# Kernel tuning notes

Hardware: AMD Instinct MI355X
Metric: run time of the kernel (lower is better)

The kernel has to match this reference:

```python
import jax, jax.numpy as jnp
import numpy as np

NEG_INF = -1.0e9  # matches torch masked_fill value of -1e9


def setup_inputs() -> dict:
    key = jax.random.key(0)
    ks = jax.random.split(key, 9)
    B, N, d, dh, de = 8, 512, 256, 64, 32
    x = jax.random.normal(ks[0], (B, N, d), dtype=jnp.float32)
    e = jax.random.normal(ks[1], (B, N, N, de), dtype=jnp.float32)
    node_mask = jax.random.randint(ks[2], (B, N), 0, 2, dtype=jnp.int32)
    Wq = jax.random.normal(ks[3], (d, dh), dtype=jnp.float32) / np.sqrt(d)
    bq = jax.random.normal(ks[4], (dh,), dtype=jnp.float32) * 0.02
    Wk = jax.random.normal(ks[5], (d, dh), dtype=jnp.float32) / np.sqrt(d)
    bk = jax.random.normal(ks[6], (dh,), dtype=jnp.float32) * 0.02
    Wv = jax.random.normal(ks[7], (d, dh), dtype=jnp.float32) / np.sqrt(d)
    bv = jax.random.normal(ks[8], (dh,), dtype=jnp.float32) * 0.02
    return {"x": x, "e": e, "node_mask": node_mask,
            "Wq": Wq, "bq": bq, "Wk": Wk, "bk": bk, "Wv": Wv, "bv": bv}


def reference(x, e, node_mask, Wq, bq, Wk, bk, Wv, bv):
    # x: (B,N,d), node_mask: (B,N) in {0,1}
    x_mask = node_mask.astype(x.dtype)[..., None]          # (B,N,1)
    Q = (x @ Wq + bq) * x_mask                              # (B,N,dh)
    K = (x @ Wk + bk) * x_mask
    V = (x @ Wv + bv) * x_mask
    sqrt_d = jnp.sqrt(jnp.asarray(Q.shape[-1], dtype=x.dtype))
    Att = jnp.einsum('bid,bjd->bij', Q, K) / sqrt_d        # (B,N,N)
    att_mask = (node_mask[:, :, None] * node_mask[:, None, :]).astype(bool)
    Att = jnp.where(att_mask, Att, NEG_INF)
    Att = jax.nn.softmax(Att, axis=-1)
    # dropout with p=0.0 is the identity
    out = jnp.einsum('bij,bjd->bid', Att, V) * x_mask       # (B,N,dh)
    return (out, e)
```

## Files before the change

kernel.cpp:

```cpp
#include <hip/hip_runtime.h>

#define B 8
#define N 512
#define D 256
#define DH 64
#define NEG_INF (-1.0e9f)
#define ROWS 8

#define ATTN_BLOCKS (B * N)
#define COPY_BLOCKS 8192
#define COPY_F4     (B * (size_t)N * N * 32 / 4)
#define COPY_ITERS  (COPY_F4 / ((size_t)COPY_BLOCKS * 256))

__global__ __launch_bounds__(192) void qkv_kernel(
    const float* __restrict__ x, const int* __restrict__ mask,
    const float* __restrict__ Wq, const float* __restrict__ bq,
    const float* __restrict__ Wk, const float* __restrict__ bk,
    const float* __restrict__ Wv, const float* __restrict__ bv,
    float* __restrict__ Q, float* __restrict__ K, float* __restrict__ V)
{
    __shared__ float xs[ROWS * D];
    const int tid  = threadIdx.x;
    const int row0 = blockIdx.x * ROWS;

    const float4* x4  = (const float4*)(x + (size_t)row0 * D);
    float4*       xs4 = (float4*)xs;
    for (int i = tid; i < ROWS * D / 4; i += 192) xs4[i] = x4[i];
    __syncthreads();

    const int which = tid >> 6;
    const int o     = tid & 63;
    const float* W    = (which == 0) ? Wq : (which == 1) ? Wk : Wv;
    const float* bias = (which == 0) ? bq : (which == 1) ? bk : bv;
    float*       Out  = (which == 0) ? Q  : (which == 1) ? K  : V;

    float acc[ROWS];
    const float bo = bias[o];
#pragma unroll
    for (int r = 0; r < ROWS; ++r) acc[r] = bo;

    for (int k = 0; k < D; ++k) {
        const float w = W[k * DH + o];
#pragma unroll
        for (int r = 0; r < ROWS; ++r)
            acc[r] += xs[r * D + k] * w;
    }

#pragma unroll
    for (int r = 0; r < ROWS; ++r) {
        const int row = row0 + r;
        const float m = (float)mask[row];
        Out[(size_t)row * DH + o] = acc[r] * m;
    }
}

__global__ __launch_bounds__(256) void fused_attn_copy(
    const float* __restrict__ Q, const float* __restrict__ K,
    const float* __restrict__ V, const int* __restrict__ mask,
    const float4* __restrict__ e4, float4* __restrict__ eout4,
    float* __restrict__ out)
{
    const int tid = threadIdx.x;

    if (blockIdx.x >= ATTN_BLOCKS) {
        const size_t stride = (size_t)COPY_BLOCKS * 256;
        size_t idx = (size_t)(blockIdx.x - ATTN_BLOCKS) * 256 + tid;
#pragma unroll
        for (int r = 0; r < (int)COPY_ITERS; ++r) {
            eout4[idx] = e4[idx];
            idx += stride;
        }
        return;
    }

    const int b = blockIdx.x >> 9;
    const int i = blockIdx.x & (N - 1);
    const int w = tid >> 6;
    const int o = tid & 63;

    __shared__ float qs[DH];
    __shared__ float sc[N];
    __shared__ float redm[4], reds[4];
    __shared__ float pv[4][DH];

    const int rowi = b * N + i;
    if (mask[rowi] == 0) {
        if (tid < DH) out[(size_t)rowi * DH + tid] = 0.0f;
        return;
    }

    if (tid < DH) qs[tid] = Q[(size_t)rowi * DH + tid];
    __syncthreads();

    float s[2];
    const float4* q4 = (const float4*)qs;
#pragma unroll
    for (int jj = 0; jj < 2; ++jj) {
        const int j = tid + jj * 256;
        const float4* k4 = (const float4*)(K + (size_t)(b * N + j) * DH);
        float acc = 0.0f;
#pragma unroll
        for (int kk = 0; kk < DH / 4; ++kk) {
            const float4 kv = k4[kk];
            const float4 qv = q4[kk];
            acc += qv.x * kv.x + qv.y * kv.y + qv.z * kv.z + qv.w * kv.w;
        }
        s[jj] = mask[b * N + j] ? acc * 0.125f : NEG_INF;
    }

    float m = fmaxf(s[0], s[1]);
#pragma unroll
    for (int off = 32; off > 0; off >>= 1)
        m = fmaxf(m, __shfl_xor(m, off));
    if (o == 0) redm[w] = m;
    __syncthreads();
    const float M = fmaxf(fmaxf(redm[0], redm[1]), fmaxf(redm[2], redm[3]));

    const float p0 = __expf(s[0] - M);
    const float p1 = __expf(s[1] - M);
    sc[tid]       = p0;
    sc[tid + 256] = p1;
    float sum = p0 + p1;
#pragma unroll
    for (int off = 32; off > 0; off >>= 1)
        sum += __shfl_xor(sum, off);
    if (o == 0) reds[w] = sum;
    __syncthreads();
    const float invSum = 1.0f / (reds[0] + reds[1] + reds[2] + reds[3]);

    float partial = 0.0f;
    const int j0 = w * 128;
    for (int j = j0; j < j0 + 128; ++j)
        partial += sc[j] * V[(size_t)(b * N + j) * DH + o];
    pv[w][o] = partial;
    __syncthreads();

    if (tid < DH) {
        const float res = (pv[0][tid] + pv[1][tid] + pv[2][tid] + pv[3][tid]) * invSum;
        out[(size_t)rowi * DH + tid] = res;
    }
}

extern "C" void kernel_launch(void* const* d_in, const int* in_sizes, int n_in,
                              void* d_out, int out_size, void* d_ws, size_t ws_size,
                              hipStream_t stream)
{
    const float* x    = (const float*)d_in[0];
    const float* e    = (const float*)d_in[1];
    const int*   mask = (const int*)  d_in[2];
    const float* Wq   = (const float*)d_in[3];
    const float* bq   = (const float*)d_in[4];
    const float* Wk   = (const float*)d_in[5];
    const float* bk   = (const float*)d_in[6];
    const float* Wv   = (const float*)d_in[7];
    const float* bv   = (const float*)d_in[8];

    float* out  = (float*)d_out;
    float* eout = out + (size_t)B * N * DH;

    float* Q = (float*)d_ws;
    float* K = Q + (size_t)B * N * DH;
    float* V = K + (size_t)B * N * DH;

    qkv_kernel<<<B * N / ROWS, 192, 0, stream>>>(x, mask, Wq, bq, Wk, bk, Wv, bv, Q, K, V);
    fused_attn_copy<<<ATTN_BLOCKS + COPY_BLOCKS, 256, 0, stream>>>(
        Q, K, V, mask, (const float4*)e, (float4*)eout, out);
}
```

Measured before the change: 539.7 us.

## Tile attention over 8 query rows per block with shared K tiles

Each attention block now handles 8 query rows instead of one. K is staged through padded shared-memory tiles and reused across the 8 rows, and each V load is shared by two rows. This cuts global K/V reads per query row and removes the early exit for masked rows, so masked rows are now computed and then zeroed. Shared memory per block grows to roughly 26KB. That also applies to the copy blocks, which may limit occupancy of the concurrent e-copy work.

```diff
diff --git a/kernel.cpp b/kernel.cpp
--- a/kernel.cpp
+++ b/kernel.cpp
@@ -7,7 +7,10 @@
 #define NEG_INF (-1.0e9f)
 #define ROWS 8
 
-#define ATTN_BLOCKS (B * N)
+#define TI 8
+#define KT 32
+#define KST 66
+#define ATTN_BLOCKS (B * N / TI)
 #define COPY_BLOCKS 8192
 #define COPY_F4     (B * (size_t)N * N * 32 / 4)
 #define COPY_ITERS  (COPY_F4 / ((size_t)COPY_BLOCKS * 256))
@@ -62,6 +65,11 @@
 {
     const int tid = threadIdx.x;
 
+    __shared__ float qs[TI][DH];
+    __shared__ float sc[TI][N];
+    __shared__ float ks[KT][KST];
+    __shared__ int   msk[N];
+
     if (blockIdx.x >= ATTN_BLOCKS) {
         const size_t stride = (size_t)COPY_BLOCKS * 256;
         size_t idx = (size_t)(blockIdx.x - ATTN_BLOCKS) * 256 + tid;
@@ -73,72 +81,72 @@
         return;
     }
 
-    const int b = blockIdx.x >> 9;
-    const int i = blockIdx.x & (N - 1);
+    const int b  = blockIdx.x >> 6;
+    const int i0 = (blockIdx.x & 63) * TI;
+
+    for (int t = tid; t < N; t += 256) msk[t] = mask[b * N + t];
+    if (tid < TI * DH / 4)
+        ((float4*)qs)[tid] = ((const float4*)(Q + (size_t)(b * N + i0) * DH))[tid];
+
+    const int jl = tid & 31;
+    const int il = tid >> 5;
+#pragma unroll 1
+    for (int jt = 0; jt < N / KT; ++jt) {
+        __syncthreads();
+        const float4* kg = (const float4*)(K + (size_t)(b * N + jt * KT) * DH);
+#pragma unroll
+        for (int u = 0; u < 2; ++u) {
+            const int g  = tid + u * 256;
+            const int jj = g >> 4;
+            const int dd = (g & 15) * 4;
+            const float4 kv = kg[g];
+            float2* dst = (float2*)&ks[jj][dd];
+            dst[0] = make_float2(kv.x, kv.y);
+            dst[1] = make_float2(kv.z, kv.w);
+        }
+        __syncthreads();
+        float acc = 0.0f;
+#pragma unroll
+        for (int k = 0; k < DH; ++k)
+            acc += qs[il][k] * ks[jl][k];
+        const int j = jt * KT + jl;
+        sc[il][j] = msk[j] ? acc * 0.125f : NEG_INF;
+    }
+    __syncthreads();
+
     const int w = tid >> 6;
     const int o = tid & 63;
-
-    __shared__ float qs[DH];
-    __shared__ float sc[N];
-    __shared__ float redm[4], reds[4];
-    __shared__ float pv[4][DH];
-
-    const int rowi = b * N + i;
-    if (mask[rowi] == 0) {
-        if (tid < DH) out[(size_t)rowi * DH + tid] = 0.0f;
-        return;
+    float inv0 = 0.0f, inv1 = 0.0f;
+#pragma unroll
+    for (int r = 0; r < 2; ++r) {
+        const int i = w + r * 4;
+        float sv[8];
+        float m = -3.402823466e38f;
+#pragma unroll
+        for (int u = 0; u < 8; ++u) { sv[u] = sc[i][o + u * 64]; m = fmaxf(m, sv[u]); }
+#pragma unroll
+        for (int off = 32; off; off >>= 1) m = fmaxf(m, __shfl_xor(m, off));
+        float sum = 0.0f;
+#pragma unroll
+        for (int u = 0; u < 8; ++u) { sv[u] = __expf(sv[u] - m); sum += sv[u]; }
+#pragma unroll
+        for (int off = 32; off; off >>= 1) sum += __shfl_xor(sum, off);
+#pragma unroll
+        for (int u = 0; u < 8; ++u) sc[i][o + u * 64] = sv[u];
+        if (r == 0) inv0 = 1.0f / sum; else inv1 = 1.0f / sum;
     }
 
-    if (tid < DH) qs[tid] = Q[(size_t)rowi * DH + tid];
-    __syncthreads();
-
-    float s[2];
-    const float4* q4 = (const float4*)qs;
-#pragma unroll
-    for (int jj = 0; jj < 2; ++jj) {
-        const int j = tid + jj * 256;
-        const float4* k4 = (const float4*)(K + (size_t)(b * N + j) * DH);
-        float acc = 0.0f;
-#pragma unroll
-        for (int kk = 0; kk < DH / 4; ++kk) {
-            const float4 kv = k4[kk];
-            const float4 qv = q4[kk];
-            acc += qv.x * kv.x + qv.y * kv.y + qv.z * kv.z + qv.w * kv.w;
-        }
-        s[jj] = mask[b * N + j] ? acc * 0.125f : NEG_INF;
+    const float* vb = V + (size_t)(b * N) * DH + o;
+    float a0 = 0.0f, a1 = 0.0f;
+#pragma unroll 8
+    for (int j = 0; j < N; ++j) {
+        const float v = vb[(size_t)j * DH];
+        a0 += sc[w][j]     * v;
+        a1 += sc[w + 4][j] * v;
     }
-
-    float m = fmaxf(s[0], s[1]);
-#pragma unroll
-    for (int off = 32; off > 0; off >>= 1)
-        m = fmaxf(m, __shfl_xor(m, off));
-    if (o == 0) redm[w] = m;
-    __syncthreads();
-    const float M = fmaxf(fmaxf(redm[0], redm[1]), fmaxf(redm[2], redm[3]));
-
-    const float p0 = __expf(s[0] - M);
-    const float p1 = __expf(s[1] - M);
-    sc[tid]       = p0;
-    sc[tid + 256] = p1;
-    float sum = p0 + p1;
-#pragma unroll
-    for (int off = 32; off > 0; off >>= 1)
-        sum += __shfl_xor(sum, off);
-    if (o == 0) reds[w] = sum;
-    __syncthreads();
-    const float invSum = 1.0f / (reds[0] + reds[1] + reds[2] + reds[3]);
-
-    float partial = 0.0f;
-    const int j0 = w * 128;
-    for (int j = j0; j < j0 + 128; ++j)
-        partial += sc[j] * V[(size_t)(b * N + j) * DH + o];
-    pv[w][o] = partial;
-    __syncthreads();
-
-    if (tid < DH) {
-        const float res = (pv[0][tid] + pv[1][tid] + pv[2][tid] + pv[3][tid]) * invSum;
-        out[(size_t)rowi * DH + tid] = res;
-    }
+    const int ra = i0 + w, rb = i0 + w + 4;
+    out[(size_t)(b * N + ra) * DH + o] = msk[ra] ? a0 * inv0 : 0.0f;
+    out[(size_t)(b * N + rb) * DH + o] = msk[rb] ? a1 * inv1 : 0.0f;
 }
 
 extern "C" void kernel_launch(void* const* d_in, const int* in_sizes, int n_in,
```

New measurement: 493.0 us. -8.7%, faster.
